# Kernel optimization log

Hardware: AMD Instinct MI355X
Metric: run time of the kernel (lower is better)

Reference implementation:

```python
import jax, jax.numpy as jnp
import numpy as np

B, S, D, H = 2, 2048, 1024, 16
DK = D // H


def setup_inputs() -> dict:
    key = jax.random.key(0)
    ks = jax.random.split(key, 12)
    scale = 1.0 / np.sqrt(D)
    inp = {
        "q": jax.random.normal(ks[0], (B, S, D), jnp.float32),
        "k": jax.random.normal(ks[1], (B, S, D), jnp.float32),
        "v": jax.random.normal(ks[2], (B, S, D), jnp.float32),
        "mask": jax.random.randint(ks[3], (B, 1, S, S), 0, 2, jnp.int32),
        "w_q": jax.random.normal(ks[4], (D, D), jnp.float32) * scale,
        "b_q": jnp.zeros((D,), jnp.float32),
        "w_k": jax.random.normal(ks[5], (D, D), jnp.float32) * scale,
        "b_k": jnp.zeros((D,), jnp.float32),
        "w_v": jax.random.normal(ks[6], (D, D), jnp.float32) * scale,
        "b_v": jnp.zeros((D,), jnp.float32),
        "w_o": jax.random.normal(ks[7], (D, D), jnp.float32) * scale,
        "b_o": jnp.zeros((D,), jnp.float32),
    }
    return inp


def reference(q, k, v, mask, w_q, b_q, w_k, b_k, w_v, b_v, w_o, b_o):
    # linear projections (torch Linear: x @ W.T + b)
    qp = q @ w_q.T + b_q  # [B,S,D]
    kp = k @ w_k.T + b_k
    vp = v @ w_v.T + b_v
    # split heads -> [B,H,S,DK]
    qh = qp.reshape(B, S, H, DK).transpose(0, 2, 1, 3)
    kh = kp.reshape(B, S, H, DK).transpose(0, 2, 1, 3)
    vh = vp.reshape(B, S, H, DK).transpose(0, 2, 1, 3)
    # scaled dot-product attention
    scores = jnp.einsum("bhqd,bhkd->bhqk", qh, kh) / jnp.sqrt(jnp.float32(DK))
    scores = jnp.where(mask == 0, jnp.float32(-1e9), scores)
    attn = jax.nn.softmax(scores, axis=-1)
    ctx = jnp.einsum("bhqk,bhkd->bhqd", attn, vh)  # [B,H,S,DK]
    ctx = ctx.transpose(0, 2, 1, 3).reshape(B, S, D)
    return ctx @ w_o.T + b_o
```

## Files before the change

### kernel.cpp

```cpp
#include <hip/hip_runtime.h>
#include <hip/hip_bf16.h>
#include <cstdint>

#define DEVINL __device__ __forceinline__

using bfrag = __attribute__((ext_vector_type(8))) __bf16;
using f32x4 = __attribute__((ext_vector_type(4))) float;
using f32x16 = __attribute__((ext_vector_type(16))) float;
using u16x4 = __attribute__((ext_vector_type(4))) unsigned short;
using u16x8 = __attribute__((ext_vector_type(8))) unsigned short;
using u32x4 = __attribute__((ext_vector_type(4))) unsigned int;

static constexpr int S_ = 2048;
static constexpr int D_ = 1024;
static constexpr int MROWS = 4096;

DEVINL unsigned short f2bf(float f) {
  __hip_bfloat16 h = __float2bfloat16(f);
  union { __hip_bfloat16 h; unsigned short u; } cv; cv.h = h; return cv.u;
}

DEVINL float fexp2(float x) {
#if __has_builtin(__builtin_amdgcn_exp2f)
  return __builtin_amdgcn_exp2f(x);
#else
  return exp2f(x);
#endif
}

DEVINL unsigned cvtpk(float lo, float hi) {
  unsigned r;
  asm("v_cvt_pk_bf16_f32 %0, %1, %2" : "=v"(r) : "v"(lo), "v"(hi));
  return r;
}

DEVINL void plswap(unsigned& x, unsigned& y) {
#if __has_builtin(__builtin_amdgcn_permlane32_swap)
  auto r = __builtin_amdgcn_permlane32_swap(x, y, false, false);
  x = r[0]; y = r[1];
#else
  unsigned px = __shfl_xor(x, 32), py = __shfl_xor(y, 32);
  bool h = (threadIdx.x & 32) != 0;
  unsigned nx = h ? py : x;
  unsigned ny = h ? y : px;
  x = nx; y = ny;
#endif
}

DEVINL void async_copy16(void* lds, const void* g) {
  __builtin_amdgcn_global_load_lds(
      (const __attribute__((address_space(1))) unsigned int*)g,
      (__attribute__((address_space(3))) unsigned int*)lds, 16, 0, 0);
}

struct CvtAll {
  const float* src[7];
  unsigned short* dst[7];
  int n4[7];
  const int* mask;
  unsigned long long* bits;
  int nmask;
};

__global__ __launch_bounds__(256) void cvt_all(CvtAll a) {
  if (blockIdx.y == 7) {
    const int n = a.nmask;
    for (int i = blockIdx.x * 256 + threadIdx.x; i < n; i += gridDim.x * 256) {
      unsigned long long b = __ballot(a.mask[i] != 0);
      if ((threadIdx.x & 63) == 0) a.bits[i >> 6] = b;
    }
    return;
  }
  const float* __restrict__ in = a.src[blockIdx.y];
  unsigned short* __restrict__ out = a.dst[blockIdx.y];
  const int n4 = a.n4[blockIdx.y];
  for (int i = blockIdx.x * 256 + threadIdx.x; i < n4; i += gridDim.x * 256) {
    f32x4 v = ((const f32x4*)in)[i];
    u16x4 o;
    o[0] = f2bf(v[0]); o[1] = f2bf(v[1]); o[2] = f2bf(v[2]); o[3] = f2bf(v[3]);
    ((u16x4*)out)[i] = o;
  }
}

template <int OMODE>
DEVINL void gemm_body(const unsigned short* __restrict__ A, const unsigned short* __restrict__ W,
                      const float* __restrict__ bias, void* __restrict__ Cout,
                      int K, int N, float oscale,
                      unsigned short* As, unsigned short* Bs, int m0, int n0) {
  const int t = threadIdx.x;
  const int lane = t & 63, wave = t >> 6;
  const int wr = wave >> 1, wc = wave & 1;
  const int g = lane >> 4, q = lane & 15;

  f32x4 acc[4][4] = {};

  const int srow = t >> 3;
  const int scol = (t & 7) * 8;
  const size_t abase = (size_t)(m0 + srow) * K + scol;
  const size_t bbase = (size_t)(n0 + srow) * K + scol;
  char* AsB = (char*)As;
  char* BsB = (char*)Bs;

  for (int k0 = 0; k0 < K; k0 += 64) {
    __syncthreads();
#pragma unroll
    for (int c = 0; c < 4; ++c) {
      async_copy16(AsB + c * 4096 + wave * 1024, A + abase + (size_t)c * 32 * K + k0);
      async_copy16(BsB + c * 4096 + wave * 1024, W + bbase + (size_t)c * 32 * K + k0);
    }
    __syncthreads();
#pragma unroll
    for (int kk = 0; kk < 64; kk += 32) {
      bfrag af[4], bf[4];
#pragma unroll
      for (int i = 0; i < 4; ++i)
        af[i] = *reinterpret_cast<const bfrag*>(&As[(wr * 64 + i * 16 + q) * 64 + kk + g * 8]);
#pragma unroll
      for (int j = 0; j < 4; ++j)
        bf[j] = *reinterpret_cast<const bfrag*>(&Bs[(wc * 64 + j * 16 + q) * 64 + kk + g * 8]);
#pragma unroll
      for (int i = 0; i < 4; ++i)
#pragma unroll
        for (int j = 0; j < 4; ++j)
          acc[i][j] = __builtin_amdgcn_mfma_f32_16x16x32_bf16(af[i], bf[j], acc[i][j], 0, 0, 0);
    }
  }

  float bv[4];
#pragma unroll
  for (int j = 0; j < 4; ++j) bv[j] = bias[n0 + wc * 64 + j * 16 + q];
#pragma unroll
  for (int i = 0; i < 4; ++i)
#pragma unroll
    for (int j = 0; j < 4; ++j) {
      int rowb = m0 + wr * 64 + i * 16 + g * 4;
      int col = n0 + wc * 64 + j * 16 + q;
      if (OMODE == 2) {
        u16x4 o;
#pragma unroll
        for (int r = 0; r < 4; ++r) o[r] = f2bf(acc[i][j][r] + bv[j]);
        *reinterpret_cast<u16x4*>(&((unsigned short*)Cout)[(size_t)col * MROWS + rowb]) = o;
      } else {
#pragma unroll
        for (int r = 0; r < 4; ++r) {
          float val = (acc[i][j][r] + bv[j]) * oscale;
          if (OMODE == 1)
            ((float*)Cout)[(size_t)(rowb + r) * N + col] = val;
          else
            ((unsigned short*)Cout)[(size_t)(rowb + r) * N + col] = f2bf(val);
        }
      }
    }
}

__global__ __launch_bounds__(256, 2) void qkv_gemm(const unsigned short* __restrict__ Abase,
                                                   const unsigned short* __restrict__ Wbase,
                                                   const float* __restrict__ b_q,
                                                   const float* __restrict__ b_k,
                                                   const float* __restrict__ b_v,
                                                   unsigned short* __restrict__ Qp,
                                                   unsigned short* __restrict__ Kp,
                                                   unsigned short* __restrict__ VpT) {
  __shared__ unsigned short As[128 * 64];
  __shared__ unsigned short Bs[128 * 64];
  const int lin = blockIdx.x + 8 * (blockIdx.y + 32 * blockIdx.z);
  const int tile = (lin & 7) * 96 + (lin >> 3);
  const int bx = tile & 7, by = (tile >> 3) & 31, z = tile >> 8;
  const unsigned short* A = Abase + (size_t)z * MROWS * D_;
  const unsigned short* W = Wbase + (size_t)z * D_ * D_;
  const int m0 = by * 128, n0 = bx * 128;
  if (z == 2) {
    gemm_body<2>(A, W, b_v, VpT, D_, D_, 1.0f, As, Bs, m0, n0);
  } else if (z == 1) {
    gemm_body<0>(A, W, b_k, Kp, D_, D_, 1.0f, As, Bs, m0, n0);
  } else {
    gemm_body<0>(A, W, b_q, Qp, D_, D_, 0.125f * 1.44269504088896340736f, As, Bs, m0, n0);
  }
}

__global__ __launch_bounds__(256, 2) void out_gemm(const unsigned short* __restrict__ A,
                                                   const unsigned short* __restrict__ W,
                                                   const float* __restrict__ bias,
                                                   float* __restrict__ out) {
  __shared__ unsigned short As[128 * 64];
  __shared__ unsigned short Bs[128 * 64];
  const int lin = blockIdx.x + 8 * blockIdx.y;
  const int tile = (lin & 7) * 32 + (lin >> 3);
  const int bx = tile & 7, by = tile >> 3;
  gemm_body<1>(A, W, bias, out, D_, D_, 1.0f, As, Bs, by * 128, bx * 128);
}

__global__ __launch_bounds__(256, 2) void attn_kernel(const unsigned short* __restrict__ Qp,
                                                      const unsigned short* __restrict__ Kp,
                                                      const unsigned short* __restrict__ VpT,
                                                      const unsigned int* __restrict__ mbits32,
                                                      unsigned short* __restrict__ ctx) {
  __shared__ unsigned short Ks[2][128 * 64];
  __shared__ unsigned short Vt[2][64 * 128];

  const int t = threadIdx.x, lane = t & 63, wave = t >> 6;
  const int hi = lane >> 5, qh = lane & 31;
  const int id = blockIdx.x + 16 * (blockIdx.y + 16 * blockIdx.z);
  const int tile = (id & 7) * 64 + (id >> 3);
  const int qt = tile & 15, bh = tile >> 4;
  const int h = bh & 15, b = bh >> 4;
  const int q0 = qt * 128;
  const int qrow = q0 + wave * 32 + qh;

  const size_t qoff = ((size_t)b * S_ + qrow) * D_ + h * 64;
  bfrag qf[4];
#pragma unroll
  for (int ks = 0; ks < 4; ++ks)
    qf[ks] = *reinterpret_cast<const bfrag*>(&Qp[qoff + ks * 16 + hi * 8]);

  f32x16 acc_o[2] = {};
  f32x16 acc_l = {};

  u16x8 onesv;
#pragma unroll
  for (int j = 0; j < 8; ++j) onesv[j] = 0x3F80;
  const bfrag ones = __builtin_bit_cast(bfrag, onesv);

  const int krow = wave * 8 + (lane >> 3);
  const int ksc = ((lane & 7) ^ (lane >> 3)) * 8;
  const size_t kbase = (size_t)b * S_ * D_ + (size_t)h * 64;
  const int vrow = wave * 4 + (lane >> 4);
  const int vsc = ((lane & 15) ^ (vrow & 7)) * 8;
  const size_t vtrow0 = (size_t)h * 64;
  const size_t vtcol0 = (size_t)b * S_;

  char* KsB = (char*)&Ks[0][0];
  char* VtB = (char*)&Vt[0][0];
  const unsigned int* mrow = mbits32 + ((size_t)b * S_ + qrow) * (S_ / 32);
  const int swz = qh & 7;

  constexpr int NT = S_ / 128;

  auto stage = [&](int buf, int ti) {
#pragma unroll
    for (int c = 0; c < 4; ++c)
      async_copy16(KsB + buf * 16384 + c * 4096 + wave * 1024,
                   &Kp[kbase + (size_t)(ti * 128 + c * 32 + krow) * D_ + ksc]);
#pragma unroll
    for (int c = 0; c < 4; ++c)
      async_copy16(VtB + buf * 16384 + c * 4096 + wave * 1024,
                   &VpT[(vtrow0 + c * 16 + vrow) * MROWS + vtcol0 + ti * 128 + vsc]);
  };

  stage(0, 0);
  __syncthreads();

  auto tile_body = [&](int ti, int cur) {
    const int nxt = cur ^ 1;
    if (ti + 1 < NT) stage(nxt, ti + 1);
    u32x4 m4 = *reinterpret_cast<const u32x4*>(mrow + ti * 4);

    f32x16 sc[4];
    const f32x16 fz = {};
    __builtin_amdgcn_s_setprio(1);
#pragma unroll
    for (int kb = 0; kb < 4; ++kb) {
#pragma unroll
      for (int ks = 0; ks < 4; ++ks) {
        bfrag kf = *reinterpret_cast<const bfrag*>(
            KsB + cur * 16384 + (kb * 32 + qh) * 128 + ((((2 * ks + hi) ^ swz) & 7) << 4));
        sc[kb] = __builtin_amdgcn_mfma_f32_32x32x16_bf16(kf, qf[ks], ks == 0 ? fz : sc[kb], 0, 0, 0);
      }
    }
    __builtin_amdgcn_s_setprio(0);

    const int sh4 = 4 * hi;
#pragma unroll
    for (int kb = 0; kb < 4; ++kb) {
      unsigned w = m4[kb] >> sh4;
#pragma unroll
      for (int g2 = 0; g2 < 4; ++g2) {
        unsigned nib = (w >> (8 * g2)) & 0xFu;
#pragma unroll
        for (int r3 = 0; r3 < 4; ++r3) {
          float p = fexp2(sc[kb][g2 * 4 + r3]);
          sc[kb][g2 * 4 + r3] = (nib & (1u << r3)) ? p : 0.f;
        }
      }
    }

    bfrag pa[8];
#pragma unroll
    for (int ks = 0; ks < 8; ++ks) {
      const int o = ks * 8;
      unsigned a1 = cvtpk(sc[(o + 0) >> 4][(o + 0) & 15], sc[(o + 1) >> 4][(o + 1) & 15]);
      unsigned a2 = cvtpk(sc[(o + 2) >> 4][(o + 2) & 15], sc[(o + 3) >> 4][(o + 3) & 15]);
      unsigned b1 = cvtpk(sc[(o + 4) >> 4][(o + 4) & 15], sc[(o + 5) >> 4][(o + 5) & 15]);
      unsigned b2 = cvtpk(sc[(o + 6) >> 4][(o + 6) & 15], sc[(o + 7) >> 4][(o + 7) & 15]);
      plswap(a1, b1);
      plswap(a2, b2);
      u32x4 wv; wv[0] = a1; wv[1] = a2; wv[2] = b1; wv[3] = b2;
      pa[ks] = __builtin_bit_cast(bfrag, wv);
    }

    __builtin_amdgcn_s_setprio(1);
#pragma unroll
    for (int ks = 0; ks < 8; ++ks) {
      acc_l = __builtin_amdgcn_mfma_f32_32x32x16_bf16(ones, pa[ks], acc_l, 0, 0, 0);
#pragma unroll
      for (int dblk = 0; dblk < 2; ++dblk) {
        bfrag va = *reinterpret_cast<const bfrag*>(
            VtB + cur * 16384 + (dblk * 32 + qh) * 256 + ((((2 * ks + hi) ^ swz) & 15) << 4));
        acc_o[dblk] = __builtin_amdgcn_mfma_f32_32x32x16_bf16(va, pa[ks], acc_o[dblk], 0, 0, 0);
      }
    }
    __builtin_amdgcn_s_setprio(0);
    __syncthreads();
  };

#pragma unroll 1
  for (int ti = 0; ti < NT; ti += 2) {
    tile_body(ti, 0);
    tile_body(ti + 1, 1);
  }

  float inv = 1.f / acc_l[0];
#pragma unroll
  for (int dblk = 0; dblk < 2; ++dblk)
#pragma unroll
    for (int g2 = 0; g2 < 4; ++g2) {
      u16x4 o;
#pragma unroll
      for (int r3 = 0; r3 < 4; ++r3) o[r3] = f2bf(acc_o[dblk][g2 * 4 + r3] * inv);
      int d0 = dblk * 32 + 8 * g2 + 4 * hi;
      *reinterpret_cast<u16x4*>(&ctx[((size_t)b * S_ + qrow) * D_ + h * 64 + d0]) = o;
    }
}

extern "C" void kernel_launch(void* const* d_in, const int* in_sizes, int n_in,
                              void* d_out, int out_size, void* d_ws, size_t ws_size,
                              hipStream_t stream) {
  const float* q = (const float*)d_in[0];
  const float* k = (const float*)d_in[1];
  const float* v = (const float*)d_in[2];
  const int* mask = (const int*)d_in[3];
  const float* w_q = (const float*)d_in[4];
  const float* b_q = (const float*)d_in[5];
  const float* w_k = (const float*)d_in[6];
  const float* b_k = (const float*)d_in[7];
  const float* w_v = (const float*)d_in[8];
  const float* b_v = (const float*)d_in[9];
  const float* w_o = (const float*)d_in[10];
  const float* b_o = (const float*)d_in[11];
  float* out = (float*)d_out;

  char* ws = (char*)d_ws;
  const size_t SZ_IN = (size_t)MROWS * D_ * 2;
  const size_t SZ_W = (size_t)D_ * D_ * 2;
  unsigned short* qb = (unsigned short*)(ws + 0);
  unsigned short* wqb = (unsigned short*)(ws + 3 * SZ_IN);
  unsigned short* wob = (unsigned short*)(ws + 3 * SZ_IN + 3 * SZ_W);
  unsigned short* Qp = (unsigned short*)(ws + 3 * SZ_IN + 4 * SZ_W);
  unsigned short* ctx = (unsigned short*)(ws + 6 * SZ_IN + 4 * SZ_W);
  unsigned long long* mbits = (unsigned long long*)(ws + 7 * SZ_IN + 4 * SZ_W);
  unsigned short* kb = qb + MROWS * D_;
  unsigned short* vb = kb + MROWS * D_;
  unsigned short* wkb = wqb + D_ * D_;
  unsigned short* wvb = wkb + D_ * D_;
  unsigned short* Kp = Qp + MROWS * D_;
  unsigned short* VpT = Kp + MROWS * D_;

  CvtAll ca;
  ca.src[0] = q;   ca.dst[0] = qb;  ca.n4[0] = MROWS * D_ / 4;
  ca.src[1] = k;   ca.dst[1] = kb;  ca.n4[1] = MROWS * D_ / 4;
  ca.src[2] = v;   ca.dst[2] = vb;  ca.n4[2] = MROWS * D_ / 4;
  ca.src[3] = w_q; ca.dst[3] = wqb; ca.n4[3] = D_ * D_ / 4;
  ca.src[4] = w_k; ca.dst[4] = wkb; ca.n4[4] = D_ * D_ / 4;
  ca.src[5] = w_v; ca.dst[5] = wvb; ca.n4[5] = D_ * D_ / 4;
  ca.src[6] = w_o; ca.dst[6] = wob; ca.n4[6] = D_ * D_ / 4;
  ca.mask = mask; ca.bits = mbits; ca.nmask = 2 * S_ * S_;
  cvt_all<<<dim3(2048, 8), 256, 0, stream>>>(ca);

  qkv_gemm<<<dim3(D_ / 128, MROWS / 128, 3), 256, 0, stream>>>(qb, wqb, b_q, b_k, b_v,
                                                               Qp, Kp, VpT);

  attn_kernel<<<dim3(S_ / 128, 16, 2), 256, 0, stream>>>(Qp, Kp, VpT,
                                                         (const unsigned int*)mbits, ctx);

  out_gemm<<<dim3(D_ / 128, MROWS / 128), 256, 0, stream>>>(ctx, wob, b_o, out);
}
```

Baseline: 133.5 us.

## Double-buffer GEMM LDS tiles and XOR-swizzle them to avoid bank conflicts

The QKV and output-projection GEMMs now use two LDS buffers. The next K-tile's async global-to-LDS copy is issued before computing on the current tile, and only one barrier is kept per iteration. The 16-byte chunks within each LDS row are also XOR-swizzled by row index to cut bank conflicts on the MFMA fragment reads. This doubles LDS use per block to 64 KB, which may limit occupancy, and leaves the attention kernel unchanged.

```diff
diff --git a/kernel.cpp b/kernel.cpp
--- a/kernel.cpp
+++ b/kernel.cpp
@@ -83,47 +83,54 @@
 }
 
 template <int OMODE>
-DEVINL void gemm_body(const unsigned short* __restrict__ A, const unsigned short* __restrict__ W,
-                      const float* __restrict__ bias, void* __restrict__ Cout,
-                      int K, int N, float oscale,
-                      unsigned short* As, unsigned short* Bs, int m0, int n0) {
+DEVINL void gemm_pipe2(const unsigned short* __restrict__ A, const unsigned short* __restrict__ W,
+                       const float* __restrict__ bias, void* __restrict__ Cout,
+                       float oscale, char* AsB, char* BsB, int m0, int n0) {
+  constexpr int K = D_, N = D_, NK = K / 64;
   const int t = threadIdx.x;
   const int lane = t & 63, wave = t >> 6;
   const int wr = wave >> 1, wc = wave & 1;
   const int g = lane >> 4, q = lane & 15;
+  const int srow = t >> 3;
+  const int sgz = (t & 7) ^ (srow & 7);
 
   f32x4 acc[4][4] = {};
 
-  const int srow = t >> 3;
-  const int scol = (t & 7) * 8;
-  const size_t abase = (size_t)(m0 + srow) * K + scol;
-  const size_t bbase = (size_t)(n0 + srow) * K + scol;
-  char* AsB = (char*)As;
-  char* BsB = (char*)Bs;
-
-  for (int k0 = 0; k0 < K; k0 += 64) {
-    __syncthreads();
+  auto stage = [&](int buf, int k0) {
 #pragma unroll
     for (int c = 0; c < 4; ++c) {
-      async_copy16(AsB + c * 4096 + wave * 1024, A + abase + (size_t)c * 32 * K + k0);
-      async_copy16(BsB + c * 4096 + wave * 1024, W + bbase + (size_t)c * 32 * K + k0);
-    }
-    __syncthreads();
+      async_copy16(AsB + buf * 16384 + c * 4096 + wave * 1024,
+                   A + (size_t)(m0 + c * 32 + srow) * K + k0 + sgz * 8);
+      async_copy16(BsB + buf * 16384 + c * 4096 + wave * 1024,
+                   W + (size_t)(n0 + c * 32 + srow) * K + k0 + sgz * 8);
+    }
+  };
+
+  stage(0, 0);
+  __syncthreads();
+
+#pragma unroll 1
+  for (int ki = 0; ki < NK; ++ki) {
+    const int cur = ki & 1;
+    if (ki + 1 < NK) stage(cur ^ 1, (ki + 1) * 64);
 #pragma unroll
     for (int kk = 0; kk < 64; kk += 32) {
       bfrag af[4], bf[4];
 #pragma unroll
       for (int i = 0; i < 4; ++i)
-        af[i] = *reinterpret_cast<const bfrag*>(&As[(wr * 64 + i * 16 + q) * 64 + kk + g * 8]);
+        af[i] = *reinterpret_cast<const bfrag*>(
+            AsB + cur * 16384 + (wr * 64 + i * 16 + q) * 128 + ((((kk >> 3) + g) ^ (q & 7)) << 4));
 #pragma unroll
       for (int j = 0; j < 4; ++j)
-        bf[j] = *reinterpret_cast<const bfrag*>(&Bs[(wc * 64 + j * 16 + q) * 64 + kk + g * 8]);
+        bf[j] = *reinterpret_cast<const bfrag*>(
+            BsB + cur * 16384 + (wc * 64 + j * 16 + q) * 128 + ((((kk >> 3) + g) ^ (q & 7)) << 4));
 #pragma unroll
       for (int i = 0; i < 4; ++i)
 #pragma unroll
         for (int j = 0; j < 4; ++j)
           acc[i][j] = __builtin_amdgcn_mfma_f32_16x16x32_bf16(af[i], bf[j], acc[i][j], 0, 0, 0);
     }
+    __syncthreads();
   }
 
   float bv[4];
@@ -161,8 +168,8 @@
                                                    unsigned short* __restrict__ Qp,
                                                    unsigned short* __restrict__ Kp,
                                                    unsigned short* __restrict__ VpT) {
-  __shared__ unsigned short As[128 * 64];
-  __shared__ unsigned short Bs[128 * 64];
+  __shared__ char As[2 * 128 * 64 * 2];
+  __shared__ char Bs[2 * 128 * 64 * 2];
   const int lin = blockIdx.x + 8 * (blockIdx.y + 32 * blockIdx.z);
   const int tile = (lin & 7) * 96 + (lin >> 3);
   const int bx = tile & 7, by = (tile >> 3) & 31, z = tile >> 8;
@@ -170,11 +177,11 @@
   const unsigned short* W = Wbase + (size_t)z * D_ * D_;
   const int m0 = by * 128, n0 = bx * 128;
   if (z == 2) {
-    gemm_body<2>(A, W, b_v, VpT, D_, D_, 1.0f, As, Bs, m0, n0);
+    gemm_pipe2<2>(A, W, b_v, VpT, 1.0f, As, Bs, m0, n0);
   } else if (z == 1) {
-    gemm_body<0>(A, W, b_k, Kp, D_, D_, 1.0f, As, Bs, m0, n0);
+    gemm_pipe2<0>(A, W, b_k, Kp, 1.0f, As, Bs, m0, n0);
   } else {
-    gemm_body<0>(A, W, b_q, Qp, D_, D_, 0.125f * 1.44269504088896340736f, As, Bs, m0, n0);
+    gemm_pipe2<0>(A, W, b_q, Qp, 0.125f * 1.44269504088896340736f, As, Bs, m0, n0);
   }
 }
 
@@ -182,12 +189,12 @@
                                                    const unsigned short* __restrict__ W,
                                                    const float* __restrict__ bias,
                                                    float* __restrict__ out) {
-  __shared__ unsigned short As[128 * 64];
-  __shared__ unsigned short Bs[128 * 64];
+  __shared__ char As[2 * 128 * 64 * 2];
+  __shared__ char Bs[2 * 128 * 64 * 2];
   const int lin = blockIdx.x + 8 * blockIdx.y;
   const int tile = (lin & 7) * 32 + (lin >> 3);
   const int bx = tile & 7, by = tile >> 3;
-  gemm_body<1>(A, W, bias, out, D_, D_, 1.0f, As, Bs, by * 128, bx * 128);
+  gemm_pipe2<1>(A, W, bias, out, 1.0f, As, Bs, by * 128, bx * 128);
 }
 
 __global__ __launch_bounds__(256, 2) void attn_kernel(const unsigned short* __restrict__ Qp,
```

Result: no change. 133.1 us (-0.4%).
